# Kernel tuning notes

Hardware: AMD Instinct MI355X
Metric: run time of the kernel (lower is better)

The kernel has to match this reference:

```python
import jax, jax.numpy as jnp
import numpy as np
from jax import lax

DN = ('NCHW', 'OIHW', 'NCHW')

def _conv(x, w, b, stride, pad):
    o = lax.conv_general_dilated(x, w, (stride, stride), [(pad, pad), (pad, pad)], dimension_numbers=DN)
    return o + b[None, :, None, None]

def _conv_transpose(x, w, b, stride, pad):
    # w in torch ConvTranspose2d layout [Cin, Cout, kh, kw]
    k = w.shape[2]
    wf = jnp.flip(w, (2, 3)).transpose(1, 0, 2, 3)  # -> [Cout, Cin, kh, kw]
    p = k - 1 - pad
    o = lax.conv_general_dilated(x, wf, (1, 1), [(p, p), (p, p)], lhs_dilation=(stride, stride), dimension_numbers=DN)
    return o + b[None, :, None, None]

def setup_inputs() -> dict:
    key = jax.random.key(0)
    ks = jax.random.split(key, 16)
    s = 0.05
    NUM_EMB, EMB_DIM = 512, 128
    inp = {
        'x': jax.random.normal(ks[0], (32, 1, 224, 224), jnp.float32),
        # encoder
        'w_e1': jax.random.normal(ks[1], (64, 1, 4, 4), jnp.float32) * s,
        'b_e1': jnp.zeros((64,), jnp.float32),
        'w_e2': jax.random.normal(ks[2], (128, 64, 4, 4), jnp.float32) * s,
        'b_e2': jnp.zeros((128,), jnp.float32),
        'w_e3': jax.random.normal(ks[3], (128, 128, 3, 3), jnp.float32) * s,
        'b_e3': jnp.zeros((128,), jnp.float32),
        # codebook (torch init: uniform(-1/K, 1/K))
        'emb': jax.random.uniform(ks[4], (NUM_EMB, EMB_DIM), jnp.float32, -1.0 / NUM_EMB, 1.0 / NUM_EMB),
        # decoder
        'w_d1': jax.random.normal(ks[5], (128, 128, 3, 3), jnp.float32) * s,
        'b_d1': jnp.zeros((128,), jnp.float32),
        'w_dt1': jax.random.normal(ks[6], (128, 64, 4, 4), jnp.float32) * s,  # ConvTranspose [Cin,Cout,k,k]
        'b_dt1': jnp.zeros((64,), jnp.float32),
        'w_dt2': jax.random.normal(ks[7], (64, 1, 4, 4), jnp.float32) * s,
        'b_dt2': jnp.zeros((1,), jnp.float32),
    }
    return inp

def reference(x, w_e1, b_e1, w_e2, b_e2, w_e3, b_e3, emb, w_d1, b_d1, w_dt1, b_dt1, w_dt2, b_dt2):
    sg = lax.stop_gradient
    # --- encoder ---
    h = jax.nn.relu(_conv(x, w_e1, b_e1, 2, 1))
    h = jax.nn.relu(_conv(h, w_e2, b_e2, 2, 1))
    z_e = _conv(h, w_e3, b_e3, 1, 1)  # [B,128,H/4,W/4]
    B, C, H, W = z_e.shape
    # --- vector quantizer (faithful to source, incl. missing -2*z@e.T cross term) ---
    z_flat = z_e.transpose(0, 2, 3, 1).reshape(-1, C)  # [BHW, C]
    distances = (z_flat ** 2).sum(1, keepdims=True) + (emb ** 2).sum(1)  # [BHW, K]
    indices = jnp.argmin(distances, axis=1)
    z_q = emb[indices].reshape(B, H, W, C).transpose(0, 3, 1, 2)
    codebook_loss = jnp.mean((z_q - sg(z_e)) ** 2)
    commitment_loss = jnp.mean((sg(z_q) - z_e) ** 2)
    vq_loss = codebook_loss + commitment_loss
    # --- decoder ---
    d = _conv(z_q, w_d1, b_d1, 1, 1)
    d = jax.nn.relu(_conv_transpose(d, w_dt1, b_dt1, 2, 1))
    reconstructed_x = _conv_transpose(d, w_dt2, b_dt2, 2, 1)
    reconstruction_loss = jnp.mean((reconstructed_x - x) ** 2)
    total_loss = reconstruction_loss + vq_loss
    return (reconstructed_x, total_loss, reconstruction_loss, vq_loss)
```

## Files before the change

### kernel.cpp

```cpp
#include <hip/hip_runtime.h>
#include <hip/hip_bf16.h>

using bf16 = __hip_bfloat16;
using short8 = __attribute__((ext_vector_type(8))) short;
using f32x16 = __attribute__((ext_vector_type(16))) float;

__device__ __forceinline__ ushort f2us(float v) {
    bf16 h = __float2bfloat16(v);
    return *reinterpret_cast<ushort*>(&h);
}

#define MFMA32(a, b, c) __builtin_amdgcn_mfma_f32_32x32x16_bf16((a), (b), (c), 0, 0, 0)

__device__ __forceinline__ void gload16(const void* g, void* l) {
    __builtin_amdgcn_global_load_lds(
        (const __attribute__((address_space(1))) unsigned int*)g,
        (__attribute__((address_space(3))) unsigned int*)l, 16, 0, 0);
}

__device__ __forceinline__ int cls8(int i) {
    if (i == 0) return 0;
    if (i == 1) return 1;
    if (i == 2) return 2;
    if (i == 109) return 5;
    if (i == 110) return 6;
    if (i == 111) return 7;
    return (i & 1) ? 4 : 3;
}

__global__ void k_codebook(const float* __restrict__ emb, float* __restrict__ c) {
    __shared__ float sval[512];
    __shared__ int   sidx[512];
    int k = threadIdx.x;
    float s = 0.f;
    const float4* e4 = (const float4*)(emb + k * 128);
    #pragma unroll
    for (int d = 0; d < 32; ++d) {
        float4 v = e4[d];
        s += v.x * v.x + v.y * v.y + v.z * v.z + v.w * v.w;
    }
    sval[k] = s; sidx[k] = k;
    __syncthreads();
    for (int off = 256; off > 0; off >>= 1) {
        if (k < off) {
            float v2 = sval[k + off]; int i2 = sidx[k + off];
            if (v2 < sval[k] || (v2 == sval[k] && i2 < sidx[k])) { sval[k] = v2; sidx[k] = i2; }
        }
        __syncthreads();
    }
    int kmin = sidx[0];
    if (k < 128) c[k] = emb[kmin * 128 + k];
}

__global__ __launch_bounds__(256) void k_prepack(const float* __restrict__ w_e2,
                                                 const float* __restrict__ w_e3,
                                                 ushort* __restrict__ Wb2f,
                                                 ushort* __restrict__ Wb3f) {
    int i = blockIdx.x * 256 + threadIdx.x;
    const int n2 = 131072;
    const int n3 = 147456;
    if (i < n2) {
        int j = i & 7, l = (i >> 3) & 63, ks = (i >> 9) & 3, mf = (i >> 11) & 1,
            mh = (i >> 12) & 1, tap = i >> 13;
        int co = mh * 64 + mf * 32 + (l & 31);
        int ci = ks * 16 + (l >> 5) * 8 + j;
        int kh = tap >> 2, kw = tap & 3;
        Wb2f[i] = f2us(w_e2[((co * 64 + ci) * 4 + kh) * 4 + kw]);
    } else if (i < n2 + n3) {
        int t = i - n2;
        int j = t & 7, l = (t >> 3) & 63, ks = (t >> 9) & 7, mf = (t >> 12) & 1,
            mh = (t >> 13) & 1, tap = t >> 14;
        int co = mh * 64 + mf * 32 + (l & 31);
        int ci = ks * 16 + (l >> 5) * 8 + j;
        int kh = tap / 3, kw = tap % 3;
        Wb3f[t] = f2us(w_e3[((co * 128 + ci) * 3 + kh) * 3 + kw]);
    }
}

__global__ __launch_bounds__(256) void k_conv1(const float* __restrict__ x,
                                               const float* __restrict__ w,
                                               const float* __restrict__ bias,
                                               ushort* __restrict__ h1s) {
    __shared__ float wl[1024];
    __shared__ float bl[64];
    __shared__ __align__(16) char obuf[28672];
    int tid = threadIdx.x;
    for (int i = tid; i < 1024; i += 256) wl[i] = w[i];
    if (tid < 64) bl[tid] = bias[tid];
    __syncthreads();
    int r = blockIdx.x, b = blockIdx.y;
    int g = tid >> 6;
    int q = tid & 63;
    bool act = q < 56;
    int oh = 2 * r + (q >= 28);
    int ow0 = (q % 28) * 4;

    float xv[4][10];
    const float* xb = x + (size_t)b * 50176;
    #pragma unroll
    for (int kh = 0; kh < 4; ++kh) {
        int ih = 2 * oh - 1 + kh;
        bool rok = act && (unsigned)ih < 224u;
        #pragma unroll
        for (int j = 0; j < 10; ++j) {
            int iw = 2 * ow0 - 1 + j;
            xv[kh][j] = (rok && (unsigned)iw < 224u) ? xb[ih * 224 + iw] : 0.f;
        }
    }
    float a[4][16];
    #pragma unroll
    for (int i = 0; i < 4; ++i)
        #pragma unroll
        for (int j = 0; j < 16; ++j) a[i][j] = 0.f;

    const float4* wl4 = (const float4*)wl;
    #pragma unroll
    for (int j = 0; j < 16; ++j) {
        int co = g * 16 + j;
        #pragma unroll
        for (int kh = 0; kh < 4; ++kh) {
            float4 wr = wl4[co * 4 + kh];
            #pragma unroll
            for (int i = 0; i < 4; ++i) {
                a[i][j] += xv[kh][2*i+0]*wr.x + xv[kh][2*i+1]*wr.y
                         + xv[kh][2*i+2]*wr.z + xv[kh][2*i+3]*wr.w;
            }
        }
    }
    if (act) {
        #pragma unroll
        for (int i = 0; i < 4; ++i) {
            int ow = ow0 + i, wq = ow >> 1, pw = ow & 1;
            char* rowb = obuf + (oh & 1) * 14336 + wq * 256;
            int key = (wq & 15) << 4;
            #pragma unroll
            for (int j = 0; j < 16; ++j) {
                int co = g * 16 + j;
                *(ushort*)(rowb + ((pw * 128 + co * 2) ^ key)) =
                    f2us(fmaxf(a[i][j] + bl[co], 0.f));
            }
        }
    }
    __syncthreads();
    const float4* sb = (const float4*)obuf;
    for (int i = tid; i < 1792; i += 256) {
        int ph = (i >= 896) ? 1 : 0;
        float4* dst = (float4*)((char*)h1s + (((size_t)(b * 2 + ph)) * 56 + r) * 14336);
        dst[i - ph * 896] = sb[i];
    }
}

#define LOADA2(buf, tp) { \
    const char* ab_ = (const char*)Wb2f + ((size_t)(((tp) * 2 + mh) * 8)) * 1024 + lane * 16; \
    _Pragma("unroll") \
    for (int mf_ = 0; mf_ < 2; ++mf_) { \
        _Pragma("unroll") \
        for (int ks_ = 0; ks_ < 4; ++ks_) \
            af[buf][mf_][ks_] = *(const short8*)(ab_ + (mf_ * 4 + ks_) * 1024); \
    } }

__global__ __launch_bounds__(512, 2) void k_conv2_mfma(const ushort* __restrict__ h1s,
                                                       const ushort* __restrict__ Wb2f,
                                                       const float* __restrict__ bias,
                                                       ushort* __restrict__ h2s) {
    __shared__ __align__(16) char ldsc[10 * 14848];
    int lin = blockIdx.x;
    int v = (lin & 7) * 56 + (lin >> 3);
    int b = v / 14, oh0 = (v % 14) * 4;
    int tid = threadIdx.x, lane = tid & 63, wv = tid >> 6;
    int mh = wv & 1, r = wv >> 1;
    int lrow = lane & 31, khalf = lane >> 5;
    const float4 z4 = {0.f, 0.f, 0.f, 0.f};

    if (tid < 320) {
        int s = tid >> 5, rr = (tid >> 4) & 1, col = tid & 15;
        ((float4*)(ldsc + s * 14848 + rr * 57 * 256))[col] = z4;
    }
    #pragma unroll
    for (int s = 0; s < 10; ++s) {
        int ph = (s < 5) ? 0 : 1;
        int rr = (s < 5) ? (oh0 + s) : (oh0 - 6 + s);
        char* ldst = ldsc + s * 14848 + 256;
        if ((unsigned)rr < 56u) {
            const char* src = (const char*)h1s + (((size_t)(b * 2 + ph)) * 56 + rr) * 14336;
            for (int c2 = wv; c2 < 14; c2 += 8)
                gload16(src + c2 * 1024 + lane * 16, ldst + c2 * 1024);
        } else {
            for (int i = tid; i < 896; i += 512) ((float4*)ldst)[i] = z4;
        }
    }
    short8 af[2][2][4];
    LOADA2(0, 0)
    LOADA2(1, 1)
    __syncthreads();

    const f32x16 vz = {0,0,0,0,0,0,0,0,0,0,0,0,0,0,0,0};
    f32x16 acc[2][2];
    #pragma unroll
    for (int cf = 0; cf < 2; ++cf)
        #pragma unroll
        for (int mf = 0; mf < 2; ++mf) acc[cf][mf] = vz;

    #pragma unroll
    for (int tap = 0; tap < 16; ++tap) {
        const int kh = tap >> 2, kw = tap & 3;
        const int pw = (kw & 1) ? 0 : 1;
        const int wofs = (kw == 0) ? 0 : (kw == 3) ? 2 : 1;
        const int sbase = (kh == 0) ? 5 : (kh == 1) ? 0 : (kh == 2) ? 6 : 1;
        const char* slab = ldsc + (sbase + r) * 14848;
        const int colb = pw * 128 + khalf * 16;
        const int cur = tap & 1;
        #pragma unroll
        for (int cf = 0; cf < 2; ++cf) {
            int wp = cf * 24 + lrow + wofs;
            int key = ((wp - 1) & 15) << 4;
            const char* rowb = slab + wp * 256;
            #pragma unroll
            for (int ks = 0; ks < 4; ++ks) {
                short8 bv = *(const short8*)(rowb + ((colb + ks * 32) ^ key));
                acc[cf][0] = MFMA32(af[cur][0][ks], bv, acc[cf][0]);
                acc[cf][1] = MFMA32(af[cur][1][ks], bv, acc[cf][1]);
            }
        }
        if (tap < 14) { LOADA2(cur, tap + 2) }
    }
    __syncthreads();
    {
        char* obuf = ldsc + r * 14336;
        #pragma unroll
        for (int cf = 0; cf < 2; ++cf) {
            int ow = cf * 24 + lrow;
            if (cf == 0 || lrow >= 8) {
                char* rowb = obuf + ow * 256;
                int key = (ow & 15) << 4;
                #pragma unroll
                for (int mf = 0; mf < 2; ++mf)
                    #pragma unroll
                    for (int reg = 0; reg < 16; ++reg) {
                        int co = mh * 64 + mf * 32 + (reg & 3) + 8 * (reg >> 2) + 4 * khalf;
                        float vv = fmaxf(acc[cf][mf][reg] + bias[co], 0.f);
                        *(ushort*)(rowb + ((co * 2) ^ key)) = f2us(vv);
                    }
            }
        }
    }
    __syncthreads();
    const float4* sb = (const float4*)ldsc;
    for (int i = tid; i < 3584; i += 512) {
        int rr = i / 896;
        float4* dst = (float4*)((char*)h2s + ((size_t)(b * 56) + oh0 + rr) * 14336);
        dst[i - rr * 896] = sb[i];
    }
}

#define LOADA3(buf, tp) { \
    const char* ab_ = (const char*)Wb3f + ((size_t)(((tp) * 2 + mh) * 16)) * 1024 + lane * 16; \
    _Pragma("unroll") \
    for (int mf_ = 0; mf_ < 2; ++mf_) { \
        _Pragma("unroll") \
        for (int ks_ = 0; ks_ < 8; ++ks_) \
            af[buf][mf_][ks_] = *(const short8*)(ab_ + (mf_ * 8 + ks_) * 1024); \
    } }

__global__ __launch_bounds__(512, 2) void k_conv3_mfma(const ushort* __restrict__ h2s,
                                                       const ushort* __restrict__ Wb3f,
                                                       const float* __restrict__ bias,
                                                       const float* __restrict__ c,
                                                       float* __restrict__ vq_part) {
    __shared__ __align__(16) char ldsc[6 * 14848];
    __shared__ float red[8];
    int lin = blockIdx.x;
    int v = (lin & 7) * 56 + (lin >> 3);
    int b = v / 14, oh0 = (v % 14) * 4;
    int tid = threadIdx.x, lane = tid & 63, wv = tid >> 6;
    int mh = wv & 1, r = wv >> 1;
    int lrow = lane & 31, khalf = lane >> 5;
    const float4 z4 = {0.f, 0.f, 0.f, 0.f};

    if (tid < 192) {
        int s = tid >> 5, rr = (tid >> 4) & 1, col = tid & 15;
        ((float4*)(ldsc + s * 14848 + rr * 57 * 256))[col] = z4;
    }
    #pragma unroll
    for (int s = 0; s < 6; ++s) {
        int rr = oh0 - 1 + s;
        char* ldst = ldsc + s * 14848 + 256;
        if ((unsigned)rr < 56u) {
            const char* src = (const char*)h2s + ((size_t)b * 56 + rr) * 14336;
            for (int c2 = wv; c2 < 14; c2 += 8)
                gload16(src + c2 * 1024 + lane * 16, ldst + c2 * 1024);
        } else {
            for (int i = tid; i < 896; i += 512) ((float4*)ldst)[i] = z4;
        }
    }
    short8 af[2][2][8];
    LOADA3(0, 0)
    LOADA3(1, 1)
    __syncthreads();

    const f32x16 vz = {0,0,0,0,0,0,0,0,0,0,0,0,0,0,0,0};
    f32x16 acc[2][2];
    #pragma unroll
    for (int cf = 0; cf < 2; ++cf)
        #pragma unroll
        for (int mf = 0; mf < 2; ++mf) acc[cf][mf] = vz;

    #pragma unroll
    for (int tap = 0; tap < 9; ++tap) {
        const int kh = tap / 3, kw = tap % 3;
        const char* slab = ldsc + (r + kh) * 14848;
        const int cur = tap & 1;
        #pragma unroll
        for (int cf = 0; cf < 2; ++cf) {
            int wp = cf * 24 + lrow + kw;
            int key = ((wp - 1) & 15) << 4;
            const char* rowb = slab + wp * 256;
            #pragma unroll
            for (int ks = 0; ks < 8; ++ks) {
                short8 bv = *(const short8*)(rowb + ((khalf * 16 + ks * 32) ^ key));
                acc[cf][0] = MFMA32(af[cur][0][ks], bv, acc[cf][0]);
                acc[cf][1] = MFMA32(af[cur][1][ks], bv, acc[cf][1]);
            }
        }
        if (tap < 7) { LOADA3(cur, tap + 2) }
    }
    float ls = 0.f;
    #pragma unroll
    for (int cf = 0; cf < 2; ++cf) {
        if (cf == 0 || lrow >= 8) {
            #pragma unroll
            for (int mf = 0; mf < 2; ++mf)
                #pragma unroll
                for (int reg = 0; reg < 16; ++reg) {
                    int co = mh * 64 + mf * 32 + (reg & 3) + 8 * (reg >> 2) + 4 * khalf;
                    float z = acc[cf][mf][reg] + bias[co];
                    float d = c[co] - z;
                    ls += d * d;
                }
        }
    }
    #pragma unroll
    for (int off = 32; off > 0; off >>= 1) ls += __shfl_down(ls, off);
    if (lane == 0) red[wv] = ls;
    __syncthreads();
    if (tid == 0) {
        float t = 0.f;
        #pragma unroll
        for (int i = 0; i < 8; ++i) t += red[i];
        vq_part[v] = t;
    }
}

__global__ __launch_bounds__(128) void k_SD3(const float* __restrict__ w_d1,
                                             const float* __restrict__ c,
                                             const float* __restrict__ b_d1,
                                             float* __restrict__ D3) {
    int co = blockIdx.x, ci = threadIdx.x;
    __shared__ float cl[128];
    __shared__ float part[9][128];
    cl[ci] = c[ci];
    __syncthreads();
    const float* wp = w_d1 + (co * 128 + ci) * 9;
    float cv = cl[ci];
    #pragma unroll
    for (int t = 0; t < 9; ++t) part[t][ci] = wp[t] * cv;
    __syncthreads();
    for (int off = 64; off > 0; off >>= 1) {
        if (ci < off) {
            #pragma unroll
            for (int t = 0; t < 9; ++t) part[t][ci] += part[t][ci + off];
        }
        __syncthreads();
    }
    if (ci < 9) {
        int rh = ci / 3, rw = ci % 3;
        int kh0 = (rh == 0) ? 1 : 0, kh1 = (rh == 2) ? 1 : 2;
        int kw0 = (rw == 0) ? 1 : 0, kw1 = (rw == 2) ? 1 : 2;
        float a = b_d1[co];
        for (int kh = kh0; kh <= kh1; ++kh)
            for (int kw = kw0; kw <= kw1; ++kw)
                a += part[kh * 3 + kw][0];
        D3[co * 9 + ci] = a;
    }
}

__global__ __launch_bounds__(64) void k_d2c(const float* __restrict__ D3,
                                            const float* __restrict__ w_dt1,
                                            const float* __restrict__ b_dt1,
                                            float* __restrict__ d2c) {
    __shared__ float dl[1152];
    int gh = blockIdx.x, gw = blockIdx.y, co2 = threadIdx.x;
    for (int i = co2; i < 1152; i += 64) dl[i] = D3[i];
    __syncthreads();
    const int rep[8] = {0, 1, 2, 4, 3, 109, 110, 111};
    int oh = rep[gh], ow = rep[gw];
    float a = b_dt1[co2];
    #pragma unroll
    for (int th = 0; th < 2; ++th) {
        int kh = ((oh + 1) & 1) + 2 * th;
        int ih = (oh + 1 - kh) >> 1;
        if ((unsigned)ih >= 56u) continue;
        int rh = (ih == 0) ? 0 : (ih == 55) ? 2 : 1;
        #pragma unroll
        for (int tw = 0; tw < 2; ++tw) {
            int kw = ((ow + 1) & 1) + 2 * tw;
            int iw = (ow + 1 - kw) >> 1;
            if ((unsigned)iw >= 56u) continue;
            int rw = (iw == 0) ? 0 : (iw == 55) ? 2 : 1;
            float t = 0.f;
            for (int ci = 0; ci < 128; ++ci)
                t += dl[ci * 9 + rh * 3 + rw] * w_dt1[(ci * 64 + co2) * 16 + kh * 4 + kw];
            a += t;
        }
    }
    d2c[(gh * 8 + gw) * 64 + co2] = fmaxf(a, 0.f);
}

__global__ __launch_bounds__(256) void k_Rbuild(const float* __restrict__ d2c,
                                                const float* __restrict__ w_dt2,
                                                const float* __restrict__ b_dt2,
                                                float* __restrict__ R) {
    __shared__ float el[1024];
    int tid = threadIdx.x;
    #pragma unroll
    for (int q = 0; q < 4; ++q) {
        int id = tid * 4 + q;
        int kh = id >> 8, kw = (id >> 6) & 3, gh = (id >> 3) & 7, gw = id & 7;
        float t = 0.f;
        const float* dp = d2c + (gh * 8 + gw) * 64;
        const float* wp = w_dt2 + kh * 4 + kw;
        for (int ci = 0; ci < 64; ++ci) t += dp[ci] * wp[ci * 16];
        el[((kh * 4 + kw) * 8 + gh) * 8 + gw] = t;
    }
    __syncthreads();
    int s = blockIdx.x * 256 + tid;
    int oh = s / 224, ow = s % 224;
    float a = b_dt2[0];
    #pragma unroll
    for (int th = 0; th < 2; ++th) {
        int kh = ((oh + 1) & 1) + 2 * th;
        int ih = (oh + 1 - kh) >> 1;
        if ((unsigned)ih >= 112u) continue;
        int ch = cls8(ih);
        #pragma unroll
        for (int tw = 0; tw < 2; ++tw) {
            int kw = ((ow + 1) & 1) + 2 * tw;
            int iw = (ow + 1 - kw) >> 1;
            if ((unsigned)iw >= 112u) continue;
            int cw = cls8(iw);
            a += el[((kh * 4 + kw) * 8 + ch) * 8 + cw];
        }
    }
    R[s] = a;
}

__global__ __launch_bounds__(256) void k_out(const float* __restrict__ R,
                                             const float* __restrict__ x,
                                             float* __restrict__ out,
                                             float* __restrict__ rec_part) {
    int base = blockIdx.x * 512 + threadIdx.x;
    float v = 0.f;
    #pragma unroll
    for (int t = 0; t < 2; ++t) {
        int i4 = base + t * 256;
        int s4 = i4 % 12544;
        float4 r = ((const float4*)R)[s4];
        float4 xv = ((const float4*)x)[i4];
        ((float4*)out)[i4] = r;
        float dx = r.x - xv.x, dy = r.y - xv.y, dz = r.z - xv.z, dw = r.w - xv.w;
        v += dx * dx + dy * dy + dz * dz + dw * dw;
    }
    __shared__ float red[4];
    #pragma unroll
    for (int off = 32; off > 0; off >>= 1) v += __shfl_down(v, off);
    int wid = threadIdx.x >> 6, lane = threadIdx.x & 63;
    if (lane == 0) red[wid] = v;
    __syncthreads();
    if (threadIdx.x == 0) rec_part[blockIdx.x] = red[0] + red[1] + red[2] + red[3];
}

__global__ __launch_bounds__(256) void k_fin(const float* __restrict__ vq_part,
                                             const float* __restrict__ rec_part,
                                             float* __restrict__ out, int loss_base) {
    __shared__ float sv[256], sr[256];
    float a = 0.f, b2 = 0.f;
    for (int i = threadIdx.x; i < 448; i += 256) a  += vq_part[i];
    for (int i = threadIdx.x; i < 784; i += 256) b2 += rec_part[i];
    sv[threadIdx.x] = a; sr[threadIdx.x] = b2;
    __syncthreads();
    for (int off = 128; off > 0; off >>= 1) {
        if (threadIdx.x < off) { sv[threadIdx.x] += sv[threadIdx.x + off]; sr[threadIdx.x] += sr[threadIdx.x + off]; }
        __syncthreads();
    }
    if (threadIdx.x == 0) {
        float vq  = 2.f * sv[0] / 12845056.f;
        float rec = sr[0] / 1605632.f;
        out[loss_base + 0] = rec + vq;
        out[loss_base + 1] = rec;
        out[loss_base + 2] = vq;
    }
}

extern "C" void kernel_launch(void* const* d_in, const int* in_sizes, int n_in,
                              void* d_out, int out_size, void* d_ws, size_t ws_size,
                              hipStream_t stream) {
    const float* x     = (const float*)d_in[0];
    const float* w_e1  = (const float*)d_in[1];
    const float* b_e1  = (const float*)d_in[2];
    const float* w_e2  = (const float*)d_in[3];
    const float* b_e2  = (const float*)d_in[4];
    const float* w_e3  = (const float*)d_in[5];
    const float* b_e3  = (const float*)d_in[6];
    const float* emb   = (const float*)d_in[7];
    const float* w_d1  = (const float*)d_in[8];
    const float* b_d1  = (const float*)d_in[9];
    const float* w_dt1 = (const float*)d_in[10];
    const float* b_dt1 = (const float*)d_in[11];
    const float* w_dt2 = (const float*)d_in[12];
    const float* b_dt2 = (const float*)d_in[13];
    float* out = (float*)d_out;
    float* ws  = (float*)d_ws;

    float* c        = ws + 16;
    float* D3       = ws + 256;
    float* d2c      = ws + 2048;
    float* R        = ws + 8192;
    float* vq_part  = ws + 65536;
    float* rec_part = ws + 67584;
    ushort* Wb2f    = (ushort*)(ws + 131072);
    ushort* Wb3f    = (ushort*)(ws + 196608);
    ushort* h1s     = (ushort*)(ws + 1310720);
    ushort* h2s     = (ushort*)(ws + 14155776);

    k_codebook<<<1, 512, 0, stream>>>(emb, c);
    k_prepack<<<1088, 256, 0, stream>>>(w_e2, w_e3, Wb2f, Wb3f);
    k_conv1<<<dim3(56, 32), 256, 0, stream>>>(x, w_e1, b_e1, h1s);
    k_conv2_mfma<<<448, 512, 0, stream>>>(h1s, Wb2f, b_e2, h2s);
    k_conv3_mfma<<<448, 512, 0, stream>>>(h2s, Wb3f, b_e3, c, vq_part);
    k_SD3<<<128, 128, 0, stream>>>(w_d1, c, b_d1, D3);
    k_d2c<<<dim3(8, 8), 64, 0, stream>>>(D3, w_dt1, b_dt1, d2c);
    k_Rbuild<<<196, 256, 0, stream>>>(d2c, w_dt2, b_dt2, R);
    k_out<<<784, 256, 0, stream>>>(R, x, out, rec_part);
    k_fin<<<1, 256, 0, stream>>>(vq_part, rec_part, out, out_size - 3);
}
```

Before: 200.9 us.

## Stage conv weight taps through double-buffered LDS and halve conv2 block tile

Weight fragments for conv2 and conv3 are no longer loaded per wave from global memory into a register double buffer. Each block now fetches one tap's weights into LDS with async global-to-LDS loads, double-buffered and with a barrier per tap, and the waves read their fragments from LDS. This cuts duplicated global weight traffic and register pressure. Conv2 is also retiled to 256-thread blocks covering two output rows, with twice as many blocks. In exchange there is a block-wide barrier on every tap, and conv3 now needs much more shared memory, which may limit how many blocks fit per CU.

```diff
diff --git a/kernel.cpp b/kernel.cpp
--- a/kernel.cpp
+++ b/kernel.cpp
@@ -150,48 +150,43 @@
     }
 }
 
-#define LOADA2(buf, tp) { \
-    const char* ab_ = (const char*)Wb2f + ((size_t)(((tp) * 2 + mh) * 8)) * 1024 + lane * 16; \
-    _Pragma("unroll") \
-    for (int mf_ = 0; mf_ < 2; ++mf_) { \
-        _Pragma("unroll") \
-        for (int ks_ = 0; ks_ < 4; ++ks_) \
-            af[buf][mf_][ks_] = *(const short8*)(ab_ + (mf_ * 4 + ks_) * 1024); \
-    } }
-
-__global__ __launch_bounds__(512, 2) void k_conv2_mfma(const ushort* __restrict__ h1s,
-                                                       const ushort* __restrict__ Wb2f,
-                                                       const float* __restrict__ bias,
-                                                       ushort* __restrict__ h2s) {
-    __shared__ __align__(16) char ldsc[10 * 14848];
+__global__ __launch_bounds__(256) void k_conv2_mfma(const ushort* __restrict__ h1s,
+                                                    const ushort* __restrict__ Wb2f,
+                                                    const float* __restrict__ bias,
+                                                    ushort* __restrict__ h2s) {
+    __shared__ __align__(16) char ldsc[6 * 14848 + 2 * 16384];
     int lin = blockIdx.x;
-    int v = (lin & 7) * 56 + (lin >> 3);
-    int b = v / 14, oh0 = (v % 14) * 4;
+    int v = (lin & 7) * 112 + (lin >> 3);
+    int b = v / 28, oh0 = (v % 28) * 2;
     int tid = threadIdx.x, lane = tid & 63, wv = tid >> 6;
     int mh = wv & 1, r = wv >> 1;
     int lrow = lane & 31, khalf = lane >> 5;
     const float4 z4 = {0.f, 0.f, 0.f, 0.f};
 
-    if (tid < 320) {
+    if (tid < 192) {
         int s = tid >> 5, rr = (tid >> 4) & 1, col = tid & 15;
         ((float4*)(ldsc + s * 14848 + rr * 57 * 256))[col] = z4;
     }
     #pragma unroll
-    for (int s = 0; s < 10; ++s) {
-        int ph = (s < 5) ? 0 : 1;
-        int rr = (s < 5) ? (oh0 + s) : (oh0 - 6 + s);
+    for (int s = 0; s < 6; ++s) {
+        int ph = (s < 3) ? 0 : 1;
+        int rr = (s < 3) ? (oh0 + s) : (oh0 - 4 + s);
         char* ldst = ldsc + s * 14848 + 256;
         if ((unsigned)rr < 56u) {
             const char* src = (const char*)h1s + (((size_t)(b * 2 + ph)) * 56 + rr) * 14336;
-            for (int c2 = wv; c2 < 14; c2 += 8)
+            for (int c2 = wv; c2 < 14; c2 += 4)
                 gload16(src + c2 * 1024 + lane * 16, ldst + c2 * 1024);
         } else {
-            for (int i = tid; i < 896; i += 512) ((float4*)ldst)[i] = z4;
-        }
-    }
-    short8 af[2][2][4];
-    LOADA2(0, 0)
-    LOADA2(1, 1)
+            for (int i = tid; i < 896; i += 256) ((float4*)ldst)[i] = z4;
+        }
+    }
+    {
+        const char* asrc = (const char*)Wb2f;
+        #pragma unroll
+        for (int t = 0; t < 4; ++t)
+            gload16(asrc + (wv * 4 + t) * 1024 + lane * 16,
+                    ldsc + 89088 + (wv * 4 + t) * 1024);
+    }
     __syncthreads();
 
     const f32x16 vz = {0,0,0,0,0,0,0,0,0,0,0,0,0,0,0,0};
@@ -203,13 +198,27 @@
 
     #pragma unroll
     for (int tap = 0; tap < 16; ++tap) {
+        const char* Acur = ldsc + 89088 + (tap & 1) * 16384;
+        if (tap < 15) {
+            char* Anxt = ldsc + 89088 + ((tap + 1) & 1) * 16384;
+            const char* asrc = (const char*)Wb2f + (size_t)(tap + 1) * 16384;
+            #pragma unroll
+            for (int t = 0; t < 4; ++t)
+                gload16(asrc + (wv * 4 + t) * 1024 + lane * 16,
+                        Anxt + (wv * 4 + t) * 1024);
+        }
+        short8 af[2][4];
+        #pragma unroll
+        for (int mf = 0; mf < 2; ++mf)
+            #pragma unroll
+            for (int ks = 0; ks < 4; ++ks)
+                af[mf][ks] = *(const short8*)(Acur + ((mh * 2 + mf) * 4 + ks) * 1024 + lane * 16);
         const int kh = tap >> 2, kw = tap & 3;
         const int pw = (kw & 1) ? 0 : 1;
         const int wofs = (kw == 0) ? 0 : (kw == 3) ? 2 : 1;
-        const int sbase = (kh == 0) ? 5 : (kh == 1) ? 0 : (kh == 2) ? 6 : 1;
+        const int sbase = (kh == 0) ? 3 : (kh == 1) ? 0 : (kh == 2) ? 4 : 1;
         const char* slab = ldsc + (sbase + r) * 14848;
         const int colb = pw * 128 + khalf * 16;
-        const int cur = tap & 1;
         #pragma unroll
         for (int cf = 0; cf < 2; ++cf) {
             int wp = cf * 24 + lrow + wofs;
@@ -218,13 +227,12 @@
             #pragma unroll
             for (int ks = 0; ks < 4; ++ks) {
                 short8 bv = *(const short8*)(rowb + ((colb + ks * 32) ^ key));
-                acc[cf][0] = MFMA32(af[cur][0][ks], bv, acc[cf][0]);
-                acc[cf][1] = MFMA32(af[cur][1][ks], bv, acc[cf][1]);
+                acc[cf][0] = MFMA32(af[0][ks], bv, acc[cf][0]);
+                acc[cf][1] = MFMA32(af[1][ks], bv, acc[cf][1]);
             }
         }
-        if (tap < 14) { LOADA2(cur, tap + 2) }
-    }
-    __syncthreads();
+        __syncthreads();
+    }
     {
         char* obuf = ldsc + r * 14336;
         #pragma unroll
@@ -246,28 +254,19 @@
     }
     __syncthreads();
     const float4* sb = (const float4*)ldsc;
-    for (int i = tid; i < 3584; i += 512) {
-        int rr = i / 896;
+    for (int i = tid; i < 1792; i += 256) {
+        int rr = (i >= 896) ? 1 : 0;
         float4* dst = (float4*)((char*)h2s + ((size_t)(b * 56) + oh0 + rr) * 14336);
         dst[i - rr * 896] = sb[i];
     }
 }
-
-#define LOADA3(buf, tp) { \
-    const char* ab_ = (const char*)Wb3f + ((size_t)(((tp) * 2 + mh) * 16)) * 1024 + lane * 16; \
-    _Pragma("unroll") \
-    for (int mf_ = 0; mf_ < 2; ++mf_) { \
-        _Pragma("unroll") \
-        for (int ks_ = 0; ks_ < 8; ++ks_) \
-            af[buf][mf_][ks_] = *(const short8*)(ab_ + (mf_ * 8 + ks_) * 1024); \
-    } }
 
 __global__ __launch_bounds__(512, 2) void k_conv3_mfma(const ushort* __restrict__ h2s,
                                                        const ushort* __restrict__ Wb3f,
                                                        const float* __restrict__ bias,
                                                        const float* __restrict__ c,
                                                        float* __restrict__ vq_part) {
-    __shared__ __align__(16) char ldsc[6 * 14848];
+    __shared__ __align__(16) char ldsc[6 * 14848 + 2 * 32768];
     __shared__ float red[8];
     int lin = blockIdx.x;
     int v = (lin & 7) * 56 + (lin >> 3);
@@ -293,9 +292,13 @@
             for (int i = tid; i < 896; i += 512) ((float4*)ldst)[i] = z4;
         }
     }
-    short8 af[2][2][8];
-    LOADA3(0, 0)
-    LOADA3(1, 1)
+    {
+        const char* asrc = (const char*)Wb3f;
+        #pragma unroll
+        for (int t = 0; t < 4; ++t)
+            gload16(asrc + (wv * 4 + t) * 1024 + lane * 16,
+                    ldsc + 89088 + (wv * 4 + t) * 1024);
+    }
     __syncthreads();
 
     const f32x16 vz = {0,0,0,0,0,0,0,0,0,0,0,0,0,0,0,0};
@@ -307,9 +310,23 @@
 
     #pragma unroll
     for (int tap = 0; tap < 9; ++tap) {
+        const char* Acur = ldsc + 89088 + (tap & 1) * 32768;
+        if (tap < 8) {
+            char* Anxt = ldsc + 89088 + ((tap + 1) & 1) * 32768;
+            const char* asrc = (const char*)Wb3f + (size_t)(tap + 1) * 32768;
+            #pragma unroll
+            for (int t = 0; t < 4; ++t)
+                gload16(asrc + (wv * 4 + t) * 1024 + lane * 16,
+                        Anxt + (wv * 4 + t) * 1024);
+        }
+        short8 af[2][8];
+        #pragma unroll
+        for (int mf = 0; mf < 2; ++mf)
+            #pragma unroll
+            for (int ks = 0; ks < 8; ++ks)
+                af[mf][ks] = *(const short8*)(Acur + ((mh * 2 + mf) * 8 + ks) * 1024 + lane * 16);
         const int kh = tap / 3, kw = tap % 3;
         const char* slab = ldsc + (r + kh) * 14848;
-        const int cur = tap & 1;
         #pragma unroll
         for (int cf = 0; cf < 2; ++cf) {
             int wp = cf * 24 + lrow + kw;
@@ -318,11 +335,11 @@
             #pragma unroll
             for (int ks = 0; ks < 8; ++ks) {
                 short8 bv = *(const short8*)(rowb + ((khalf * 16 + ks * 32) ^ key));
-                acc[cf][0] = MFMA32(af[cur][0][ks], bv, acc[cf][0]);
-                acc[cf][1] = MFMA32(af[cur][1][ks], bv, acc[cf][1]);
+                acc[cf][0] = MFMA32(af[0][ks], bv, acc[cf][0]);
+                acc[cf][1] = MFMA32(af[1][ks], bv, acc[cf][1]);
             }
         }
-        if (tap < 7) { LOADA3(cur, tap + 2) }
+        __syncthreads();
     }
     float ls = 0.f;
     #pragma unroll
@@ -535,7 +552,7 @@
     k_codebook<<<1, 512, 0, stream>>>(emb, c);
     k_prepack<<<1088, 256, 0, stream>>>(w_e2, w_e3, Wb2f, Wb3f);
     k_conv1<<<dim3(56, 32), 256, 0, stream>>>(x, w_e1, b_e1, h1s);
-    k_conv2_mfma<<<448, 512, 0, stream>>>(h1s, Wb2f, b_e2, h2s);
+    k_conv2_mfma<<<896, 256, 0, stream>>>(h1s, Wb2f, b_e2, h2s);
     k_conv3_mfma<<<448, 512, 0, stream>>>(h2s, Wb3f, b_e3, c, vq_part);
     k_SD3<<<128, 128, 0, stream>>>(w_d1, c, b_d1, D3);
     k_d2c<<<dim3(8, 8), 64, 0, stream>>>(D3, w_dt1, b_dt1, d2c);
```

After: 185.7 us. 1.08x faster.
